# Optimization experiments

Hardware: AMD Instinct MI355X
Metric: run time of the kernel (lower is better)

Reference implementation:

```python
import jax, jax.numpy as jnp
import numpy as np

B, N, E, K, H = 4, 2048, 512, 16, 8
EMB = 2 * E  # MultiheadAttention embed_dim = input_enc * 2


def setup_inputs() -> dict:
    key = jax.random.key(0)
    ks = jax.random.split(key, 6)
    s = 0.02
    return {
        "x": jax.random.normal(ks[0], (B, N, E), jnp.float32),
        "x_enc": jax.random.normal(ks[1], (B, N, EMB), jnp.float32),
        "w_in": jax.random.normal(ks[2], (3 * EMB, EMB), jnp.float32) * s,
        "b_in": jnp.zeros((3 * EMB,), jnp.float32),
        "w_out": jax.random.normal(ks[3], (EMB, EMB), jnp.float32) * s,
        "b_out": jnp.zeros((EMB,), jnp.float32),
        "k": K,
    }


def _knn_mean(x, k):
    # x: (B, N, E). torch code transposes to (B, E, N) and treats the E channel
    # rows as the 'points' for kNN (distance matrix is (B, E, E)).
    xt = jnp.swapaxes(x, 1, 2)                      # (B, E, N)
    sq = jnp.sum(xt * xt, axis=-1)                  # (B, E)
    dist = sq[:, :, None] + sq[:, None, :] - 2.0 * jnp.einsum("ben,bfn->bef", xt, xt)
    idx = jax.lax.top_k(-dist, k)[1]                # (B, E, k) smallest distances
    # fused gather + mean: avoid the (B, E, E, N) expand from the torch code
    nbrs = jnp.take_along_axis(xt[:, None, :, :], idx[:, :, :, None], axis=2)  # (B, E, k, N)
    return jnp.swapaxes(jnp.mean(nbrs, axis=2), 1, 2)  # (B, N, E)


def _mha(q, kv, w_in, b_in, w_out, b_out, h):
    # faithful torch nn.MultiheadAttention (batch_first) forward
    wq, wk, wv = jnp.split(w_in, 3, axis=0)
    bq, bk, bv = jnp.split(b_in, 3, axis=0)
    Q = q @ wq.T + bq
    Kt = kv @ wk.T + bk
    V = kv @ wv.T + bv
    b, l, emb = Q.shape
    m = Kt.shape[1]
    d = emb // h

    def split_heads(t):
        return t.reshape(t.shape[0], t.shape[1], h, d).transpose(0, 2, 1, 3)

    Qh, Kh, Vh = split_heads(Q), split_heads(Kt), split_heads(V)
    scores = jnp.einsum("bhld,bhmd->bhlm", Qh, Kh) / jnp.sqrt(jnp.float32(d))
    att = jax.nn.softmax(scores, axis=-1)
    o = jnp.einsum("bhlm,bhmd->bhld", att, Vh)      # (B, H, L, d)
    o = o.transpose(0, 2, 1, 3).reshape(b, l, emb)
    return o @ w_out.T + b_out


def reference(x, x_enc, w_in, b_in, w_out, b_out, k):
    b, n, e = x.shape
    x_knn = _knn_mean(x, k)                          # (B, N, E)
    cat = jnp.concatenate([jnp.swapaxes(x, 1, 2), jnp.swapaxes(x_knn, 1, 2)], axis=-1)  # (B, E, 2N)
    # faithful to torch .view(-1, 2*E, N): row-interleaving reshape, NOT a transpose
    q = jnp.swapaxes(cat.reshape(b, 2 * e, n), 1, 2)  # (B, N, 2E)
    attn = _mha(q, x_enc, w_in, b_in, w_out, b_out, H)  # (B, N, 2E)
    return jnp.concatenate([q, attn], axis=1)         # (B, 2N, 2E)
```

## Files before the change

### kernel.cpp

```cpp
#include <hip/hip_runtime.h>
#include <hip/hip_bf16.h>

#define B_ 4
#define N_ 2048
#define E_ 512
#define EMB_ 1024
#define H_ 8
#define D_ 128
#define KNN_ 16

typedef short short8_t __attribute__((ext_vector_type(8)));
typedef short short4_t __attribute__((ext_vector_type(4)));
typedef float float2_t __attribute__((ext_vector_type(2)));
typedef float float4_t __attribute__((ext_vector_type(4)));
typedef float float16_t __attribute__((ext_vector_type(16)));
typedef unsigned int uint2_t __attribute__((ext_vector_type(2)));
typedef unsigned int uint4_t __attribute__((ext_vector_type(4)));

__device__ __forceinline__ short f2bf(float f) {
  unsigned u = __float_as_uint(f);
  unsigned r = u + 0x7fffu + ((u >> 16) & 1u);
  return (short)(r >> 16);
}

__device__ __forceinline__ unsigned pk2bf(float a, float b) {
  float2 f; f.x = a; f.y = b;
  __hip_bfloat162 h = __float22bfloat162_rn(f);
  return *(unsigned*)&h;
}

__device__ __forceinline__ float fexp2(float x) {
  return __builtin_amdgcn_exp2f(x);
}

__device__ __forceinline__ void gload16(const short* g, short* l) {
  __builtin_amdgcn_global_load_lds(
      (const __attribute__((address_space(1))) void*)g,
      (__attribute__((address_space(3))) void*)l, 16, 0, 0);
}

__global__ __launch_bounds__(256) void k_sqnp_part(const float* __restrict__ x,
                                                   float* __restrict__ part) {
  const int t = blockIdx.x * 256 + threadIdx.x;
  if (t >= B_ * E_ * 16) return;
  const int be = t & (B_ * E_ - 1), blk = t >> 11;
  const int b = be >> 9, e = be & (E_ - 1);
  const float* p = x + (size_t)b * N_ * E_ + (size_t)blk * 128 * E_ + e;
  float lane[16];
#pragma unroll
  for (int l = 0; l < 16; l++) {
    float pr[8];
#pragma unroll
    for (int j = 0; j < 8; j++) {
      float v = p[(size_t)(j * 16 + l) * E_];
      pr[j] = __fmul_rn(v, v);
    }
    float s01 = __fadd_rn(pr[0], pr[1]);
    float s23 = __fadd_rn(pr[2], pr[3]);
    float s45 = __fadd_rn(pr[4], pr[5]);
    float s67 = __fadd_rn(pr[6], pr[7]);
    lane[l] = __fadd_rn(__fadd_rn(s01, s23), __fadd_rn(s45, s67));
  }
  float bb[8];
#pragma unroll
  for (int l = 0; l < 8; l++) bb[l] = __fadd_rn(lane[l], lane[l + 8]);
  float cc[4];
#pragma unroll
  for (int l = 0; l < 4; l++) cc[l] = __fadd_rn(bb[l], bb[l + 4]);
  part[(size_t)be * 16 + blk] =
      __fadd_rn(__fadd_rn(cc[0], cc[1]), __fadd_rn(cc[2], cc[3]));
}

__global__ __launch_bounds__(256) void k_sqnp_fin(const float* __restrict__ part,
                                                  float* __restrict__ sq) {
  const int t = blockIdx.x * 256 + threadIdx.x;
  if (t >= B_ * E_) return;
  const float* bs = part + (size_t)t * 16;
  float t1[8], t2[4];
#pragma unroll
  for (int l = 0; l < 8; l++) t1[l] = __fadd_rn(bs[2 * l], bs[2 * l + 1]);
#pragma unroll
  for (int l = 0; l < 4; l++) t2[l] = __fadd_rn(t1[2 * l], t1[2 * l + 1]);
  sq[t] = __fadd_rn(__fadd_rn(t2[0], t2[1]), __fadd_rn(t2[2], t2[3]));
}

__global__ __launch_bounds__(64) void k_gram_sym(const float* __restrict__ x,
                                                 float* __restrict__ g) {
  __shared__ __align__(16) float Xs[2][32][68];
  const int bx = blockIdx.x;
  int p = bx >> 1;
  const int jh = bx & 1;
  const int b = blockIdx.y;
  int ti = 0;
  while (p >= 16 - ti) { p -= 16 - ti; ti++; }
  const int tj = ti + p;
  const int i0 = ti * 32, j0 = tj * 32 + jh * 16;
  const int lane = threadIdx.x;
  const int li = lane & 7, lj = lane >> 3;
  const int cq = lane & 7, rn = lane >> 3;
  const int qj = lane & 3, rj = lane >> 2;
  const float* xb = x + (size_t)b * N_ * E_;

  float acc[4][2];
#pragma unroll
  for (int u = 0; u < 4; u++) { acc[u][0] = 0.f; acc[u][1] = 0.f; }

  float4_t gi[4], gj[2];
#pragma unroll
  for (int ps = 0; ps < 4; ps++) {
    const int n = ps * 8 + rn;
    gi[ps] = *(const float4_t*)(xb + (size_t)n * E_ + i0 + cq * 4);
  }
#pragma unroll
  for (int s = 0; s < 2; s++) {
    const int n = s * 16 + rj;
    gj[s] = *(const float4_t*)(xb + (size_t)n * E_ + j0 + qj * 4);
  }
#pragma unroll
  for (int ps = 0; ps < 4; ps++) {
    const int nn = ps * 8 + rn;
    *(float4_t*)&Xs[0][nn][(cq * 4) ^ ((nn & 7) << 2)] = gi[ps];
  }
#pragma unroll
  for (int s = 0; s < 2; s++) {
    const int nn = s * 16 + rj;
    *(float4_t*)&Xs[0][nn][32 + ((qj * 4) ^ ((nn & 3) << 2))] = gj[s];
  }

  for (int c = 0; c < 64; c++) {
    const int buf = c & 1;
    if (c < 63) {
      const int nb = (c + 1) * 32;
#pragma unroll
      for (int ps = 0; ps < 4; ps++) {
        const int n = nb + ps * 8 + rn;
        gi[ps] = *(const float4_t*)(xb + (size_t)n * E_ + i0 + cq * 4);
      }
#pragma unroll
      for (int s = 0; s < 2; s++) {
        const int n = nb + s * 16 + rj;
        gj[s] = *(const float4_t*)(xb + (size_t)n * E_ + j0 + qj * 4);
      }
    }
#pragma unroll
    for (int nn = 0; nn < 32; nn++) {
      const float4_t va = *(const float4_t*)
          &Xs[buf][nn][(li * 4) ^ ((nn & 7) << 2)];
      const float2_t vb = *(const float2_t*)
          &Xs[buf][nn][32 + (((lj >> 1) * 4) ^ ((nn & 3) << 2)) + (lj & 1) * 2];
#pragma unroll
      for (int u = 0; u < 4; u++) {
        acc[u][0] = __fadd_rn(acc[u][0], __fmul_rn(va[u], vb[0]));
        acc[u][1] = __fadd_rn(acc[u][1], __fmul_rn(va[u], vb[1]));
      }
    }
    if (c < 63) {
#pragma unroll
      for (int ps = 0; ps < 4; ps++) {
        const int nn = ps * 8 + rn;
        *(float4_t*)&Xs[buf ^ 1][nn][(cq * 4) ^ ((nn & 7) << 2)] = gi[ps];
      }
#pragma unroll
      for (int s = 0; s < 2; s++) {
        const int nn = s * 16 + rj;
        *(float4_t*)&Xs[buf ^ 1][nn][32 + ((qj * 4) ^ ((nn & 3) << 2))] = gj[s];
      }
    }
  }
  float* gb = g + (size_t)b * E_ * E_;
#pragma unroll
  for (int u = 0; u < 4; u++) {
#pragma unroll
    for (int v = 0; v < 2; v++) {
      const int i = i0 + li * 4 + u, j = j0 + lj * 2 + v;
      gb[(size_t)i * E_ + j] = acc[u][v];
      if (ti != tj) gb[(size_t)j * E_ + i] = acc[u][v];
    }
  }
}

__global__ __launch_bounds__(64) void k_topk(const float* __restrict__ sq,
                                             const float* __restrict__ g,
                                             int* __restrict__ idxout) {
  const int bi = blockIdx.x;
  const int b = bi >> 9, i = bi & (E_ - 1);
  const int lane = threadIdx.x;
  const float* gb = g + ((size_t)b * E_ + i) * E_;
  const float* sqb = sq + ((size_t)b << 9);
  const float sqi = sqb[i];
  const int base = lane * 8;
  float v[8];
#pragma unroll
  for (int u = 0; u < 8; u++) {
    v[u] = __fsub_rn(__fadd_rn(sqi, sqb[base + u]),
                     __fmul_rn(2.0f, gb[base + u]));
  }
  for (int t = 0; t < KNN_; t++) {
    float best = 3.0e38f; int bidx = E_;
#pragma unroll
    for (int u = 0; u < 8; u++) {
      if (v[u] < best) { best = v[u]; bidx = base + u; }
    }
#pragma unroll
    for (int off = 1; off < 64; off <<= 1) {
      float ov = __shfl_xor(best, off);
      int oi = __shfl_xor(bidx, off);
      if (ov < best || (ov == best && oi < bidx)) { best = ov; bidx = oi; }
    }
    if (lane == 0) idxout[(size_t)bi * KNN_ + t] = bidx;
#pragma unroll
    for (int u = 0; u < 8; u++) {
      if (bidx == base + u) v[u] = 3.0e38f;
    }
  }
}

__global__ __launch_bounds__(256) void k_knnmean(const float* __restrict__ x,
                                                 const int* __restrict__ idx,
                                                 float* __restrict__ out,
                                                 short* __restrict__ Xq) {
  const int n = blockIdx.x, b = blockIdx.y;
  const int tid = threadIdx.x;
  __shared__ float xrow[E_];
  const float* xr = x + ((size_t)b * N_ + n) * E_;
  for (int i = tid; i < E_; i += 256) xrow[i] = xr[i];
  __syncthreads();
  float* orow = out + ((size_t)b * (2 * N_) + n) * EMB_;
  unsigned* qrow = (unsigned*)(Xq + ((size_t)b * N_ + n) * EMB_);
  for (int i = tid; i < E_; i += 256) {
    const int* id = idx + ((size_t)b * E_ + i) * KNN_;
    float s = 0.f;
#pragma unroll
    for (int t = 0; t < KNN_; t++) s = __fadd_rn(s, xrow[id[t]]);
    float2 w; w.x = xrow[i]; w.y = s * (1.0f / 16.0f);
    *(float2*)&orow[2 * i] = w;
    qrow[i] = pk2bf(w.x, w.y);
  }
}

__global__ __launch_bounds__(256) void k_cvt(const float* __restrict__ src,
                                             short* __restrict__ dst, int n8) {
  const int t = blockIdx.x * 256 + threadIdx.x;
  if (t >= n8) return;
  const float* s = src + (size_t)t * 8;
  float4 a = *(const float4*)s, b = *(const float4*)(s + 4);
  short8_t v;
  v[0] = f2bf(a.x); v[1] = f2bf(a.y); v[2] = f2bf(a.z); v[3] = f2bf(a.w);
  v[4] = f2bf(b.x); v[5] = f2bf(b.y); v[6] = f2bf(b.z); v[7] = f2bf(b.w);
  *(short8_t*)(dst + (size_t)t * 8) = v;
}

__global__ __launch_bounds__(256) void k_gemm_qkv(
    const short* __restrict__ Xq, const short* __restrict__ Xe,
    const short* __restrict__ Win, const float* __restrict__ b_in,
    short* __restrict__ Qb, short* __restrict__ Kb, short* __restrict__ Vb) {
  __shared__ __align__(16) short As[128 * 64];
  __shared__ __align__(16) short Bs[128 * 64];
  const int tid = threadIdx.x;
  const int z = blockIdx.z;
  const short* X = (z == 0) ? Xq : Xe;
  const short* W = Win + (size_t)z * EMB_ * EMB_;
  const float* bias = b_in + z * EMB_;
  const int row0 = blockIdx.x * 128, col0 = blockIdx.y * 128;
  const int l = tid & 63, lg = l >> 4, lq = l & 15;
  const int w = tid >> 6, wm = w >> 1, wn = w & 1;
  float4_t acc[4][4];
#pragma unroll
  for (int i = 0; i < 4; i++)
#pragma unroll
    for (int j = 0; j < 4; j++) {
      acc[i][j][0] = 0.f; acc[i][j][1] = 0.f; acc[i][j][2] = 0.f; acc[i][j][3] = 0.f;
    }

  int soff[4], ldsb[4];
#pragma unroll
  for (int ii = 0; ii < 4; ii++) {
    const int cid = ii * 256 + tid;
    const int r = cid >> 3, c = cid & 7;
    soff[ii] = r * EMB_ + ((c * 8) ^ ((r & 7) << 3));
    ldsb[ii] = (ii * 256 + w * 64) * 8;
  }
  const short* Xb = X + (size_t)row0 * EMB_;
  const short* Wb = W + (size_t)col0 * EMB_;

  for (int kt = 0; kt < 16; kt++) {
    __syncthreads();
#pragma unroll
    for (int ii = 0; ii < 4; ii++) {
      gload16(Xb + soff[ii] + kt * 64, As + ldsb[ii]);
      gload16(Wb + soff[ii] + kt * 64, Bs + ldsb[ii]);
    }
    __syncthreads();
#pragma unroll
    for (int kk = 0; kk < 2; kk++) {
      short8_t af[4], bf[4];
#pragma unroll
      for (int mi = 0; mi < 4; mi++) {
        const int r = wm * 64 + mi * 16 + lq;
        af[mi] = *(const short8_t*)&As[r * 64 + ((kk * 32 + lg * 8) ^ ((r & 7) << 3))];
      }
#pragma unroll
      for (int ni = 0; ni < 4; ni++) {
        const int r = wn * 64 + ni * 16 + lq;
        bf[ni] = *(const short8_t*)&Bs[r * 64 + ((kk * 32 + lg * 8) ^ ((r & 7) << 3))];
      }
#pragma unroll
      for (int mi = 0; mi < 4; mi++)
#pragma unroll
        for (int ni = 0; ni < 4; ni++)
          acc[mi][ni] = __builtin_amdgcn_mfma_f32_16x16x32_bf16(af[mi], bf[ni], acc[mi][ni], 0, 0, 0);
    }
  }
  short* Yb = (z == 0) ? Qb : ((z == 1) ? Kb : Vb);
#pragma unroll
  for (int ni = 0; ni < 4; ni++) {
    const int col = col0 + wn * 64 + ni * 16 + lq;
    const float bv = bias[col];
#pragma unroll
    for (int mi = 0; mi < 4; mi++) {
#pragma unroll
      for (int j = 0; j < 4; j++) {
        const int m = row0 + wm * 64 + mi * 16 + lg * 4 + j;
        const float v = acc[mi][ni][j] + bv;
        if (z < 2) {
          Yb[(size_t)m * EMB_ + col] = f2bf(v);
        } else {
          const int b2 = m >> 11, n2 = m & (N_ - 1);
          Yb[((size_t)b2 * EMB_ + col) * N_ + n2] = f2bf(v);
        }
      }
    }
  }
}

__global__ __launch_bounds__(256) void k_gemm_out(
    const short* __restrict__ X, const short* __restrict__ W,
    const float* __restrict__ bias, float* __restrict__ Yf) {
  __shared__ __align__(16) short As[128 * 64];
  __shared__ __align__(16) short Bs[128 * 64];
  const int tid = threadIdx.x;
  const int row0 = blockIdx.x * 128, col0 = blockIdx.y * 128;
  const int l = tid & 63, lg = l >> 4, lq = l & 15;
  const int w = tid >> 6, wm = w >> 1, wn = w & 1;
  float4_t acc[4][4];
#pragma unroll
  for (int i = 0; i < 4; i++)
#pragma unroll
    for (int j = 0; j < 4; j++) {
      acc[i][j][0] = 0.f; acc[i][j][1] = 0.f; acc[i][j][2] = 0.f; acc[i][j][3] = 0.f;
    }

  int soff[4], ldsb[4];
#pragma unroll
  for (int ii = 0; ii < 4; ii++) {
    const int cid = ii * 256 + tid;
    const int r = cid >> 3, c = cid & 7;
    soff[ii] = r * EMB_ + ((c * 8) ^ ((r & 7) << 3));
    ldsb[ii] = (ii * 256 + w * 64) * 8;
  }
  const short* Xb = X + (size_t)row0 * EMB_;
  const short* Wb = W + (size_t)col0 * EMB_;

  for (int kt = 0; kt < 16; kt++) {
    __syncthreads();
#pragma unroll
    for (int ii = 0; ii < 4; ii++) {
      gload16(Xb + soff[ii] + kt * 64, As + ldsb[ii]);
      gload16(Wb + soff[ii] + kt * 64, Bs + ldsb[ii]);
    }
    __syncthreads();
#pragma unroll
    for (int kk = 0; kk < 2; kk++) {
      short8_t af[4], bf[4];
#pragma unroll
      for (int mi = 0; mi < 4; mi++) {
        const int r = wm * 64 + mi * 16 + lq;
        af[mi] = *(const short8_t*)&As[r * 64 + ((kk * 32 + lg * 8) ^ ((r & 7) << 3))];
      }
#pragma unroll
      for (int ni = 0; ni < 4; ni++) {
        const int r = wn * 64 + ni * 16 + lq;
        bf[ni] = *(const short8_t*)&Bs[r * 64 + ((kk * 32 + lg * 8) ^ ((r & 7) << 3))];
      }
#pragma unroll
      for (int mi = 0; mi < 4; mi++)
#pragma unroll
        for (int ni = 0; ni < 4; ni++)
          acc[mi][ni] = __builtin_amdgcn_mfma_f32_16x16x32_bf16(af[mi], bf[ni], acc[mi][ni], 0, 0, 0);
    }
  }
#pragma unroll
  for (int ni = 0; ni < 4; ni++) {
    const int col = col0 + wn * 64 + ni * 16 + lq;
    const float bv = bias[col];
#pragma unroll
    for (int mi = 0; mi < 4; mi++) {
#pragma unroll
      for (int j = 0; j < 4; j++) {
        const int m = row0 + wm * 64 + mi * 16 + lg * 4 + j;
        const int b2 = m >> 11, n2 = m & (N_ - 1);
        Yf[((size_t)b2 * 2 * N_ + N_ + n2) * EMB_ + col] = acc[mi][ni][j] + bv;
      }
    }
  }
}

__global__ __launch_bounds__(256, 2) void k_flash_bf16(
    const short* __restrict__ Qg, const short* __restrict__ Kg,
    const short* __restrict__ Vtg, short* __restrict__ Og) {
  __shared__ __align__(16) short Ks[64 * 128];
  __shared__ __align__(16) short Vs[128 * 64];
  const int tid = threadIdx.x;
  const int w = tid >> 6, l = tid & 63;
  const int hi = l >> 5, l5 = l & 31;
  const int bid = blockIdx.x;
  const int bh = (bid & 7) * 4 + ((bid >> 3) >> 4);
  const int rt = (bid >> 3) & 15;
  const int b = bh >> 3, h = bh & 7;
  const float c1 = 0.08838834764831845f * 1.4426950408889634f;
  const size_t bhoff = (size_t)b * N_ * EMB_ + (size_t)h * D_;
  const int ksw = (l5 & 15) << 3;
  const int psw = (l5 & 7) << 3;

  int koff[4], vofs[4], klds[4], vlds[4];
#pragma unroll
  for (int ii = 0; ii < 4; ii++) {
    const int cid = ii * 256 + tid;
    const int kr = cid >> 4, kc = cid & 15;
    const int vr = cid >> 3, vc = cid & 7;
    koff[ii] = kr * EMB_ + kc * 8;
    vofs[ii] = vr * N_ + vc * 8;
    klds[ii] = kr * 128 + ((kc * 8) ^ ((kr & 15) << 3));
    vlds[ii] = vr * 64 + ((vc * 8) ^ ((vr & 7) << 3));
  }
  const short* Kt0 = Kg + bhoff;
  const short* Vt0 = Vtg + (size_t)b * EMB_ * N_ + (size_t)(h * D_) * N_;

  short8_t qf[8];
  {
    const short* qrow = Qg + bhoff + (size_t)(rt * 128 + w * 32 + l5) * EMB_;
#pragma unroll
    for (int s = 0; s < 8; s++)
      qf[s] = *(const short8_t*)(qrow + s * 16 + hi * 8);
  }
  float16_t oacc[4];
#pragma unroll
  for (int dg = 0; dg < 4; dg++)
#pragma unroll
    for (int r = 0; r < 16; r++) oacc[dg][r] = 0.f;
  float m = -3.0e38f, lsum = 0.f;

  short8_t kreg[4], vreg[4];
#pragma unroll
  for (int ii = 0; ii < 4; ii++) {
    kreg[ii] = *(const short8_t*)(Kt0 + koff[ii]);
    vreg[ii] = *(const short8_t*)(Vt0 + vofs[ii]);
  }
#pragma unroll
  for (int ii = 0; ii < 4; ii++) {
    *(short8_t*)&Ks[klds[ii]] = kreg[ii];
    *(short8_t*)&Vs[vlds[ii]] = vreg[ii];
  }
  __syncthreads();

  for (int kt = 0; kt < N_ / 64; kt++) {
    if (kt + 1 < N_ / 64) {
      const short* Kt = Kt0 + (size_t)((kt + 1) * 64) * EMB_;
      const short* Vt = Vt0 + (kt + 1) * 64;
#pragma unroll
      for (int ii = 0; ii < 4; ii++) {
        kreg[ii] = *(const short8_t*)(Kt + koff[ii]);
        vreg[ii] = *(const short8_t*)(Vt + vofs[ii]);
      }
    }

    float16_t s0, s1;
#pragma unroll
    for (int r = 0; r < 16; r++) { s0[r] = 0.f; s1[r] = 0.f; }
    __builtin_amdgcn_s_setprio(1);
#pragma unroll
    for (int s = 0; s < 8; s++) {
      const int col = (s * 16 + hi * 8) ^ ksw;
      short8_t kf0 = *(const short8_t*)&Ks[l5 * 128 + col];
      short8_t kf1 = *(const short8_t*)&Ks[(32 + l5) * 128 + col];
      s0 = __builtin_amdgcn_mfma_f32_32x32x16_bf16(kf0, qf[s], s0, 0, 0, 0);
      s1 = __builtin_amdgcn_mfma_f32_32x32x16_bf16(kf1, qf[s], s1, 0, 0, 0);
    }
    __builtin_amdgcn_s_setprio(0);

    float tm = s0[0];
#pragma unroll
    for (int r = 1; r < 16; r++) tm = fmaxf(tm, s0[r]);
#pragma unroll
    for (int r = 0; r < 16; r++) tm = fmaxf(tm, s1[r]);
    tm = fmaxf(tm, __shfl_xor(tm, 32));
    if (__any(tm > m + 62.7f)) {
      const float mn = fmaxf(m, tm);
      const float alpha = fexp2((m - mn) * c1);
      m = mn;
      lsum *= alpha;
#pragma unroll
      for (int dg = 0; dg < 4; dg++)
#pragma unroll
        for (int r = 0; r < 16; r++) oacc[dg][r] *= alpha;
    }
    const float mc1 = m * c1;
    float ps = 0.f;
    unsigned w0[8], w1[8];
#pragma unroll
    for (int t = 0; t < 4; t++) {
      float p0 = fexp2(__builtin_fmaf(s0[4 * t + 0], c1, -mc1));
      float p1 = fexp2(__builtin_fmaf(s0[4 * t + 1], c1, -mc1));
      float p2 = fexp2(__builtin_fmaf(s0[4 * t + 2], c1, -mc1));
      float p3 = fexp2(__builtin_fmaf(s0[4 * t + 3], c1, -mc1));
      ps += (p0 + p1) + (p2 + p3);
      w0[t] = pk2bf(p0, p1); w1[t] = pk2bf(p2, p3);
    }
#pragma unroll
    for (int t = 0; t < 4; t++) {
      float p0 = fexp2(__builtin_fmaf(s1[4 * t + 0], c1, -mc1));
      float p1 = fexp2(__builtin_fmaf(s1[4 * t + 1], c1, -mc1));
      float p2 = fexp2(__builtin_fmaf(s1[4 * t + 2], c1, -mc1));
      float p3 = fexp2(__builtin_fmaf(s1[4 * t + 3], c1, -mc1));
      ps += (p0 + p1) + (p2 + p3);
      w0[4 + t] = pk2bf(p0, p1); w1[4 + t] = pk2bf(p2, p3);
    }
    ps += __shfl_xor(ps, 32);
    lsum += ps;

    short8_t pf[4];
#pragma unroll
    for (int ks = 0; ks < 4; ks++) {
      const int t0 = 2 * ks, t1 = 2 * ks + 1;
      uint2_t ra = __builtin_amdgcn_permlane32_swap(w0[t0], w0[t1], false, false);
      uint2_t rb = __builtin_amdgcn_permlane32_swap(w1[t0], w1[t1], false, false);
      uint4_t pw; pw[0] = ra[0]; pw[1] = rb[0]; pw[2] = ra[1]; pw[3] = rb[1];
      pf[ks] = *(short8_t*)&pw;
    }

    __builtin_amdgcn_s_setprio(1);
#pragma unroll
    for (int ks = 0; ks < 4; ks++) {
      const int col = (ks * 16 + hi * 8) ^ psw;
#pragma unroll
      for (int dg = 0; dg < 4; dg++) {
        short8_t vf = *(const short8_t*)&Vs[(dg * 32 + l5) * 64 + col];
        oacc[dg] = __builtin_amdgcn_mfma_f32_32x32x16_bf16(vf, pf[ks], oacc[dg], 0, 0, 0);
      }
    }
    __builtin_amdgcn_s_setprio(0);

    __syncthreads();
    if (kt + 1 < N_ / 64) {
#pragma unroll
      for (int ii = 0; ii < 4; ii++) {
        *(short8_t*)&Ks[klds[ii]] = kreg[ii];
        *(short8_t*)&Vs[vlds[ii]] = vreg[ii];
      }
      __syncthreads();
    }
  }

  const float linv = 1.0f / lsum;
  short* orow = Og + bhoff + (size_t)(rt * 128 + w * 32 + l5) * EMB_;
#pragma unroll
  for (int dg = 0; dg < 4; dg++) {
#pragma unroll
    for (int g = 0; g < 4; g++) {
      float p0 = oacc[dg][4 * g + 0] * linv;
      float p1 = oacc[dg][4 * g + 1] * linv;
      float p2 = oacc[dg][4 * g + 2] * linv;
      float p3 = oacc[dg][4 * g + 3] * linv;
      uint2 ow; ow.x = pk2bf(p0, p1); ow.y = pk2bf(p2, p3);
      *(uint2*)&orow[dg * 32 + g * 8 + hi * 4] = ow;
    }
  }
}

extern "C" void kernel_launch(void* const* d_in, const int* in_sizes, int n_in,
                              void* d_out, int out_size, void* d_ws, size_t ws_size,
                              hipStream_t stream) {
  const float* x     = (const float*)d_in[0];
  const float* x_enc = (const float*)d_in[1];
  const float* w_in  = (const float*)d_in[2];
  const float* b_in  = (const float*)d_in[3];
  const float* w_out = (const float*)d_in[4];
  const float* b_out = (const float*)d_in[5];
  float* out = (float*)d_out;
  char* wsb = (char*)d_ws;

  const size_t oG    = 0;
  const size_t oSq   = oG + (size_t)B_ * E_ * E_ * 4;
  const size_t oPart = oSq + (size_t)B_ * E_ * 4;
  const size_t oIdx  = oPart + (size_t)B_ * E_ * 16 * 4;
  const size_t oXq   = (oIdx + (size_t)B_ * E_ * KNN_ * 4 + 255) & ~(size_t)255;
  const size_t sB    = (size_t)B_ * N_ * EMB_ * 2;
  const size_t oXe   = oXq + sB;
  const size_t oWin  = oXe + sB;
  const size_t oWo   = oWin + 3ull * EMB_ * EMB_ * 2;
  const size_t oQ    = oWo + (size_t)EMB_ * EMB_ * 2;
  const size_t oK    = oQ + sB;
  const size_t oV    = oK + sB;
  const size_t oO    = oV + sB;
  const size_t need  = oO + sB;

  float* g    = (float*)(wsb + oG);
  float* sqv  = (float*)(wsb + oSq);
  float* part = (float*)(wsb + oPart);
  int*   idx  = (int*)(wsb + oIdx);
  short* Xq   = (short*)(wsb + oXq);
  short* Xe   = (short*)(wsb + oXe);
  short* Win  = (short*)(wsb + oWin);
  short* Wo   = (short*)(wsb + oWo);
  short* Qb   = (short*)(wsb + oQ);
  short* Kb   = (short*)(wsb + oK);
  short* Vb   = (short*)(wsb + oV);
  short* Ob   = (ws_size >= need) ? (short*)(wsb + oO) : Qb;

  k_sqnp_part<<<dim3(B_ * E_ * 16 / 256), 256, 0, stream>>>(x, part);
  k_sqnp_fin<<<dim3(B_ * E_ / 256), 256, 0, stream>>>(part, sqv);
  k_gram_sym<<<dim3(272, B_), 64, 0, stream>>>(x, g);
  k_topk<<<dim3(B_ * E_), 64, 0, stream>>>(sqv, g, idx);
  k_knnmean<<<dim3(N_, B_), 256, 0, stream>>>(x, idx, out, Xq);

  k_cvt<<<dim3(4096), 256, 0, stream>>>(x_enc, Xe, B_ * N_ * EMB_ / 8);
  k_cvt<<<dim3(1536), 256, 0, stream>>>(w_in, Win, 3 * EMB_ * EMB_ / 8);
  k_cvt<<<dim3(512), 256, 0, stream>>>(w_out, Wo, EMB_ * EMB_ / 8);

  k_gemm_qkv<<<dim3(64, 8, 3), 256, 0, stream>>>(Xq, Xe, Win, b_in, Qb, Kb, Vb);

  k_flash_bf16<<<dim3(512), 256, 0, stream>>>(Qb, Kb, Vb, Ob);

  k_gemm_out<<<dim3(64, 8), 256, 0, stream>>>(Ob, Wo, b_out, out);
}
```

Before: 324.5 us.

## Double-buffer flash attention K/V tiles with direct global-to-LDS loads

The flash-attention kernel now keeps two LDS buffers for the K and V tiles. The next tile is fetched straight from global memory into the alternate buffer with gload16, instead of staging it through registers and then writing it to LDS. The XOR swizzle moves from the LDS write address to the global source address, so the MFMA read pattern stays the same. This drops one __syncthreads and the register copy per iteration, and lets the loads overlap the MFMA work. In exchange it doubles LDS use per block, and correctness depends on the async loads finishing before the barrier.

```diff
diff --git a/kernel.cpp b/kernel.cpp
--- a/kernel.cpp
+++ b/kernel.cpp
@@ -408,8 +408,8 @@
 __global__ __launch_bounds__(256, 2) void k_flash_bf16(
     const short* __restrict__ Qg, const short* __restrict__ Kg,
     const short* __restrict__ Vtg, short* __restrict__ Og) {
-  __shared__ __align__(16) short Ks[64 * 128];
-  __shared__ __align__(16) short Vs[128 * 64];
+  __shared__ __align__(16) short Ks[2][64 * 128];
+  __shared__ __align__(16) short Vs[2][128 * 64];
   const int tid = threadIdx.x;
   const int w = tid >> 6, l = tid & 63;
   const int hi = l >> 5, l5 = l & 31;
@@ -422,16 +422,15 @@
   const int ksw = (l5 & 15) << 3;
   const int psw = (l5 & 7) << 3;
 
-  int koff[4], vofs[4], klds[4], vlds[4];
+  int ksrc[4], vsrc[4], ldb[4];
 #pragma unroll
   for (int ii = 0; ii < 4; ii++) {
     const int cid = ii * 256 + tid;
     const int kr = cid >> 4, kc = cid & 15;
     const int vr = cid >> 3, vc = cid & 7;
-    koff[ii] = kr * EMB_ + kc * 8;
-    vofs[ii] = vr * N_ + vc * 8;
-    klds[ii] = kr * 128 + ((kc * 8) ^ ((kr & 15) << 3));
-    vlds[ii] = vr * 64 + ((vc * 8) ^ ((vr & 7) << 3));
+    ksrc[ii] = kr * EMB_ + ((kc * 8) ^ ((kr & 15) << 3));
+    vsrc[ii] = vr * N_ + ((vc * 8) ^ ((vr & 7) << 3));
+    ldb[ii] = (ii * 256 + w * 64) * 8;
   }
   const short* Kt0 = Kg + bhoff;
   const short* Vt0 = Vtg + (size_t)b * EMB_ * N_ + (size_t)(h * D_) * N_;
@@ -450,27 +449,22 @@
     for (int r = 0; r < 16; r++) oacc[dg][r] = 0.f;
   float m = -3.0e38f, lsum = 0.f;
 
-  short8_t kreg[4], vreg[4];
 #pragma unroll
   for (int ii = 0; ii < 4; ii++) {
-    kreg[ii] = *(const short8_t*)(Kt0 + koff[ii]);
-    vreg[ii] = *(const short8_t*)(Vt0 + vofs[ii]);
-  }
-#pragma unroll
-  for (int ii = 0; ii < 4; ii++) {
-    *(short8_t*)&Ks[klds[ii]] = kreg[ii];
-    *(short8_t*)&Vs[vlds[ii]] = vreg[ii];
+    gload16(Kt0 + ksrc[ii], &Ks[0][ldb[ii]]);
+    gload16(Vt0 + vsrc[ii], &Vs[0][ldb[ii]]);
   }
   __syncthreads();
 
   for (int kt = 0; kt < N_ / 64; kt++) {
+    const int buf = kt & 1;
     if (kt + 1 < N_ / 64) {
       const short* Kt = Kt0 + (size_t)((kt + 1) * 64) * EMB_;
       const short* Vt = Vt0 + (kt + 1) * 64;
 #pragma unroll
       for (int ii = 0; ii < 4; ii++) {
-        kreg[ii] = *(const short8_t*)(Kt + koff[ii]);
-        vreg[ii] = *(const short8_t*)(Vt + vofs[ii]);
+        gload16(Kt + ksrc[ii], &Ks[buf ^ 1][ldb[ii]]);
+        gload16(Vt + vsrc[ii], &Vs[buf ^ 1][ldb[ii]]);
       }
     }
 
@@ -481,8 +475,8 @@
 #pragma unroll
     for (int s = 0; s < 8; s++) {
       const int col = (s * 16 + hi * 8) ^ ksw;
-      short8_t kf0 = *(const short8_t*)&Ks[l5 * 128 + col];
-      short8_t kf1 = *(const short8_t*)&Ks[(32 + l5) * 128 + col];
+      short8_t kf0 = *(const short8_t*)&Ks[buf][l5 * 128 + col];
+      short8_t kf1 = *(const short8_t*)&Ks[buf][(32 + l5) * 128 + col];
       s0 = __builtin_amdgcn_mfma_f32_32x32x16_bf16(kf0, qf[s], s0, 0, 0, 0);
       s1 = __builtin_amdgcn_mfma_f32_32x32x16_bf16(kf1, qf[s], s1, 0, 0, 0);
     }
@@ -544,21 +538,13 @@
       const int col = (ks * 16 + hi * 8) ^ psw;
 #pragma unroll
       for (int dg = 0; dg < 4; dg++) {
-        short8_t vf = *(const short8_t*)&Vs[(dg * 32 + l5) * 64 + col];
+        short8_t vf = *(const short8_t*)&Vs[buf][(dg * 32 + l5) * 64 + col];
         oacc[dg] = __builtin_amdgcn_mfma_f32_32x32x16_bf16(vf, pf[ks], oacc[dg], 0, 0, 0);
       }
     }
     __builtin_amdgcn_s_setprio(0);
 
     __syncthreads();
-    if (kt + 1 < N_ / 64) {
-#pragma unroll
-      for (int ii = 0; ii < 4; ii++) {
-        *(short8_t*)&Ks[klds[ii]] = kreg[ii];
-        *(short8_t*)&Vs[vlds[ii]] = vreg[ii];
-      }
-      __syncthreads();
-    }
   }
 
   const float linv = 1.0f / lsum;
```

Result: no change. 324.2 us (-0.1%).
